# Optimization experiments

Hardware: AMD Instinct MI355X
Metric: run time of the kernel (lower is better)

Reference implementation:

```python
import jax, jax.numpy as jnp
import numpy as np

L, I, H = 4, 256, 512          # layers, input_size, hidden_size
SH, LH, GH = 4, 2, 2            # short/long/global heads
NH, HD, FF = SH + LH + GH, H // (SH + LH + GH), 2 * H
S, B = 1024, 8                  # seq (AST nodes), batch
EPS = 1e-5
NEG = -1e9


def _ln(x, g, b):
    m = jnp.mean(x, axis=-1, keepdims=True)
    v = jnp.var(x, axis=-1, keepdims=True)
    return (x - m) * jax.lax.rsqrt(v + EPS) * g + b


def setup_inputs() -> dict:
    key = jax.random.key(0)
    ks = jax.random.split(key, 10)
    w = lambda k, shape: jax.random.normal(k, shape, jnp.float32) * 0.02
    return {
        "nodes": jax.random.normal(ks[0], (S, B, I), jnp.float32),
        "dist": jax.random.randint(ks[1], (B, S, S), 0, 5, jnp.int32),
        "dense_w": w(ks[2], (H, I)), "dense_b": jnp.zeros((H,), jnp.float32),
        "dense_ln_g": jnp.ones((H,), jnp.float32), "dense_ln_b": jnp.zeros((H,), jnp.float32),
        "qkv_w": w(ks[3], (L, 3 * H, H)), "qkv_b": jnp.zeros((L, 3 * H), jnp.float32),
        "out_w": w(ks[4], (L, H, H)), "out_b": jnp.zeros((L, H), jnp.float32),
        "ln1_g": jnp.ones((L, H), jnp.float32), "ln1_b": jnp.zeros((L, H), jnp.float32),
        "ffn_w1": w(ks[5], (L, FF, H)), "ffn_b1": jnp.zeros((L, FF), jnp.float32),
        "ffn_w2": w(ks[6], (L, H, FF)), "ffn_b2": jnp.zeros((L, H), jnp.float32),
        "ln2_g": jnp.ones((L, H), jnp.float32), "ln2_b": jnp.zeros((L, H), jnp.float32),
        "bn_g": jnp.ones((H,), jnp.float32), "bn_b": jnp.zeros((H,), jnp.float32),
    }


def _mask_bias(dist):
    # dist: [B,S,S] int -> additive bias [B,NH,S,S]
    short = (dist == 1)[:, None]                       # [B,1,S,S]
    longm = (dist >= 1)[:, None]
    globm = jnp.broadcast_to((dist[:, 0:1, :] >= 1)[:, None], (dist.shape[0], 1, S, S))
    allowed = jnp.concatenate([
        jnp.broadcast_to(short, (dist.shape[0], SH, S, S)),
        jnp.broadcast_to(longm, (dist.shape[0], LH, S, S)),
        jnp.broadcast_to(globm, (dist.shape[0], GH, S, S)),
    ], axis=1)
    allowed = allowed | jnp.eye(S, dtype=bool)
    return jnp.where(allowed, 0.0, NEG).astype(jnp.float32)


def _forward(nodes, dist, dense_w, dense_b, dense_ln_g, dense_ln_b,
             qkv_w, qkv_b, out_w, out_b, ln1_g, ln1_b,
             ffn_w1, ffn_b1, ffn_w2, ffn_b2, ln2_g, ln2_b, bn_g, bn_b):
    x = jnp.transpose(nodes, (1, 0, 2))                # [B,S,I]
    x = _ln(x @ dense_w.T + dense_b, dense_ln_g, dense_ln_b)  # [B,S,H]
    bias = _mask_bias(dist)                            # [B,NH,S,S]
    scale = 1.0 / np.sqrt(HD)

    def layer(x, p):
        (wqkv, bqkv, wo, bo, g1, b1, w1, bf1, w2, bf2, g2, b2) = p
        qkv = x @ wqkv.T + bqkv                        # [B,S,3H]
        q, k, v = jnp.split(qkv, 3, axis=-1)
        q = q.reshape(B, S, NH, HD).transpose(0, 2, 1, 3)
        k = k.reshape(B, S, NH, HD).transpose(0, 2, 1, 3)
        v = v.reshape(B, S, NH, HD).transpose(0, 2, 1, 3)
        scores = jnp.einsum('bhqd,bhkd->bhqk', q, k) * scale + bias
        attn = jax.nn.softmax(scores, axis=-1)
        o = jnp.einsum('bhqk,bhkd->bhqd', attn, v)
        o = o.transpose(0, 2, 1, 3).reshape(B, S, H) @ wo.T + bo
        x = _ln(x + o, g1, b1)
        f = jax.nn.relu(x @ w1.T + bf1) @ w2.T + bf2
        x = _ln(x + f, g2, b2)
        return x, None

    params = (qkv_w, qkv_b, out_w, out_b, ln1_g, ln1_b,
              ffn_w1, ffn_b1, ffn_w2, ffn_b2, ln2_g, ln2_b)
    x, _ = jax.lax.scan(layer, x, params)
    hidden = x[:, 0]                                   # first token -> [B,H]
    m = jnp.mean(hidden, axis=0)
    v = jnp.var(hidden, axis=0)
    return (hidden - m) * jax.lax.rsqrt(v + EPS) * bn_g + bn_b


def reference(nodes, dist, dense_w, dense_b, dense_ln_g, dense_ln_b,
              qkv_w, qkv_b, out_w, out_b, ln1_g, ln1_b,
              ffn_w1, ffn_b1, ffn_w2, ffn_b2, ln2_g, ln2_b, bn_g, bn_b):
    return _forward(nodes, dist, dense_w, dense_b, dense_ln_g, dense_ln_b,
                    qkv_w, qkv_b, out_w, out_b, ln1_g, ln1_b,
                    ffn_w1, ffn_b1, ffn_w2, ffn_b2, ln2_g, ln2_b, bn_g, bn_b)
```

## Files before the change

### kernel.cpp

```cpp
#include <hip/hip_runtime.h>
#include <hip/hip_bf16.h>
#include <math.h>

#define LAYERS 4
#define IDIM 256
#define HDIM 512
#define NH 8
#define HD 64
#define FF 1024
#define SEQ 1024
#define BATCH 8
#define EPS 1e-5f

typedef __attribute__((ext_vector_type(8))) short short8;
typedef __attribute__((ext_vector_type(4))) short short4v;
typedef __attribute__((ext_vector_type(4))) float f32x4;
typedef unsigned long long u64;

__device__ __forceinline__ short f2bf(float f) {
    unsigned u = __float_as_uint(f);
    u = (u + 0x7FFFu + ((u >> 16) & 1u)) >> 16;
    return (short)u;
}
__device__ __forceinline__ float bf2f(short s) {
    return __uint_as_float(((unsigned)(unsigned short)s) << 16);
}
__device__ __forceinline__ void gll16(const void* g, void* l) {
    __builtin_amdgcn_global_load_lds(
        (const __attribute__((address_space(1))) unsigned int*)g,
        (__attribute__((address_space(3))) unsigned int*)l, 16, 0, 0);
}

__global__ __launch_bounds__(256) void cvt_bf16(const float* __restrict__ in,
                                                short* __restrict__ out) {
    size_t i = ((size_t)blockIdx.x * 256 + threadIdx.x) * 4;
    f32x4 f = *(const f32x4*)(in + i);
    short4v o = {f2bf(f[0]), f2bf(f[1]), f2bf(f[2]), f2bf(f[3])};
    *(short4v*)(out + i) = o;
}

__global__ __launch_bounds__(256) void transpose_nodes(const float* __restrict__ nodes,
                                                       short* __restrict__ xt) {
    size_t idx = ((size_t)blockIdx.x * 256 + threadIdx.x) * 4;
    int i  = idx & (IDIM - 1);
    int sb = idx >> 8;
    int b  = sb & (BATCH - 1);
    int s  = sb >> 3;
    f32x4 f = *(const f32x4*)(nodes + idx);
    short4v o = {f2bf(f[0]), f2bf(f[1]), f2bf(f[2]), f2bf(f[3])};
    *(short4v*)(xt + ((size_t)b * SEQ + s) * IDIM + i) = o;
}

__global__ __launch_bounds__(256) void build_masks(const int* __restrict__ dist,
                                                   u64* __restrict__ mS,
                                                   u64* __restrict__ mL,
                                                   u64* __restrict__ mG) {
    int t = blockIdx.x * 256 + threadIdx.x;
    int w = t & 15, q = (t >> 4) & 1023, b = t >> 14;
    const int* dp = dist + ((size_t)b * SEQ + q) * SEQ + w * 64;
    u64 bs = 0, bl = 0;
    for (int i = 0; i < 64; i++) {
        int d = dp[i];
        bs |= (u64)(d == 1) << i;
        bl |= (u64)(d >= 1) << i;
    }
    mS[((size_t)b * SEQ + q) * 16 + w] = bs;
    mL[((size_t)b * SEQ + q) * 16 + w] = bl;
    if (q == 0) mG[b * 16 + w] = bl;
}

template<int BM>
__global__ __launch_bounds__(256, 2)
void gemm_bf16(const short* __restrict__ A, const short* __restrict__ W,
               const float* __restrict__ bias, short* __restrict__ C,
               int M, int N, int K, int relu) {
    __shared__ __align__(16) short As[BM * 64];
    __shared__ __align__(16) short Ws[128 * 64];
    const int tid = threadIdx.x;
    const int w = tid >> 6, lane = tid & 63;
    const int l15 = lane & 15, quad = lane >> 4;
    const int m0 = blockIdx.y * BM, n0 = blockIdx.x * 128;

    constexpr int NI = (BM == 128) ? 4 : 2;
    const int wm = (BM == 128) ? (w >> 1) * 64 : 0;
    const int wn = (BM == 128) ? (w & 1) * 64 : w * 32;

    f32x4 acc[4][NI];
#pragma unroll
    for (int mi = 0; mi < 4; mi++)
#pragma unroll
        for (int ni = 0; ni < NI; ni++) acc[mi][ni] = (f32x4){0.f, 0.f, 0.f, 0.f};

    const int r_in = lane >> 3;
    const int c8   = lane & 7;

    for (int k0 = 0; k0 < K; k0 += 64) {
#pragma unroll
        for (int rep = 0; rep < BM * 8 / 256; rep++) {
            int chunk = rep * 4 + w;
            int row = chunk * 8 + r_in;
            const short* src = A + (size_t)(m0 + row) * K + k0 + ((c8 ^ (row & 7)) << 3);
            gll16(src, (char*)As + chunk * 1024);
        }
#pragma unroll
        for (int rep = 0; rep < 4; rep++) {
            int chunk = rep * 4 + w;
            int row = chunk * 8 + r_in;
            const short* src = W + (size_t)(n0 + row) * K + k0 + ((c8 ^ (row & 7)) << 3);
            gll16(src, (char*)Ws + chunk * 1024);
        }
        __syncthreads();
#pragma unroll
        for (int ks = 0; ks < 2; ks++) {
            short8 af[4], wf[NI];
            const int dblk = ks * 4 + quad;
#pragma unroll
            for (int mi = 0; mi < 4; mi++) {
                int row = wm + mi * 16 + l15;
                af[mi] = *(const short8*)((const char*)As + row * 128 + ((dblk ^ (row & 7)) << 4));
            }
#pragma unroll
            for (int ni = 0; ni < NI; ni++) {
                int row = wn + ni * 16 + l15;
                wf[ni] = *(const short8*)((const char*)Ws + row * 128 + ((dblk ^ (row & 7)) << 4));
            }
#pragma unroll
            for (int mi = 0; mi < 4; mi++)
#pragma unroll
                for (int ni = 0; ni < NI; ni++)
                    acc[mi][ni] = __builtin_amdgcn_mfma_f32_16x16x32_bf16(
                        af[mi], wf[ni], acc[mi][ni], 0, 0, 0);
        }
        __syncthreads();
    }
#pragma unroll
    for (int ni = 0; ni < NI; ni++) {
        int n = n0 + wn + ni * 16 + l15;
        float bz = bias[n];
#pragma unroll
        for (int mi = 0; mi < 4; mi++) {
#pragma unroll
            for (int r = 0; r < 4; r++) {
                int m = m0 + wm + mi * 16 + quad * 4 + r;
                float v = acc[mi][ni][r] + bz;
                if (relu) v = fmaxf(v, 0.f);
                C[(size_t)m * N + n] = f2bf(v);
            }
        }
    }
}

__global__ __launch_bounds__(256) void v_transpose(const short* __restrict__ qkv,
                                                   short* __restrict__ vt) {
    const int s0 = blockIdx.x * 64, h = blockIdx.y, b = blockIdx.z;
    __shared__ __align__(16) short T[64 * 72];
    const int tid = threadIdx.x;
#pragma unroll
    for (int rep = 0; rep < 2; rep++) {
        int item = tid + rep * 256;
        int sl = item >> 3, c = item & 7;
        short8 v = *(const short8*)(qkv + ((size_t)(b * SEQ + s0 + sl) * 1536) + 1024 + h * 64 + c * 8);
        *(short8*)(T + sl * 72 + c * 8) = v;
    }
    __syncthreads();
    int d = tid & 63, g = tid >> 6;
    short8 o0, o1;
#pragma unroll
    for (int i = 0; i < 8; i++) o0[i] = T[(g * 16 + i) * 72 + d];
#pragma unroll
    for (int i = 0; i < 8; i++) o1[i] = T[(g * 16 + 8 + i) * 72 + d];
    short* dst = vt + ((size_t)((b * NH + h) * HD + d) * SEQ) + s0 + g * 16;
    *(short8*)dst = o0;
    *(short8*)(dst + 8) = o1;
}

#define EXP2SC 0.18033688011112042f
__global__ __launch_bounds__(256, 3)
void attn_mfma(const short* __restrict__ qkv, const short* __restrict__ vt,
               const u64* __restrict__ maskS, const u64* __restrict__ maskL,
               const u64* __restrict__ maskG, short* __restrict__ out) {
    const int tid = threadIdx.x;
    const int w = tid >> 6, lane = tid & 63, l15 = lane & 15, quad = lane >> 4;
    const int p = blockIdx.x;
    const int g_ = (p & 7) + 8 * (p >> 7);
    const int qt = (p >> 3) & 15;
    const int b = g_ >> 3, h = g_ & 7;
    const int q = qt * 64 + w * 16 + l15;

    __shared__ __align__(16) short Ks[64 * 64];
    __shared__ __align__(16) short Vs[64 * 64];

    short8 qf[2];
    {
        const short* qrow = qkv + ((size_t)(b * SEQ + q) * 1536) + h * 64;
#pragma unroll
        for (int ks = 0; ks < 2; ks++)
            qf[ks] = *(const short8*)(qrow + ks * 32 + quad * 8);
    }
    const u64* mrow = (h < 4) ? (maskS + ((size_t)b * SEQ + q) * 16)
                   : (h < 6) ? (maskL + ((size_t)b * SEQ + q) * 16)
                   :           (maskG + (size_t)b * 16);

    f32x4 of[4];
#pragma unroll
    for (int mt = 0; mt < 4; mt++) of[mt] = (f32x4){0.f, 0.f, 0.f, 0.f};
    float lsum = 0.f;

    const int r_in = lane >> 3, c8 = lane & 7;
    for (int kt = 0; kt < SEQ; kt += 64) {
#pragma unroll
        for (int rep = 0; rep < 2; rep++) {
            int chunk = rep * 4 + w;
            int row = chunk * 8 + r_in;
            const short* ksrc = qkv + ((size_t)(b * SEQ + kt + row) * 1536) + 512 + h * 64 + ((c8 ^ (row & 7)) << 3);
            gll16(ksrc, (char*)Ks + chunk * 1024);
            const short* vsrc = vt + ((size_t)((b * NH + h) * HD + row) * SEQ) + kt + ((c8 ^ (row & 7)) << 3);
            gll16(vsrc, (char*)Vs + chunk * 1024);
        }
        __syncthreads();

        f32x4 sa[4];
#pragma unroll
        for (int g = 0; g < 4; g++) sa[g] = (f32x4){0.f, 0.f, 0.f, 0.f};
#pragma unroll
        for (int ks = 0; ks < 2; ks++) {
            const int dblk = ks * 4 + quad;
#pragma unroll
            for (int g = 0; g < 4; g++) {
                int row = g * 16 + l15;
                short8 kf = *(const short8*)((const char*)Ks + row * 128 + ((dblk ^ (row & 7)) << 4));
                sa[g] = __builtin_amdgcn_mfma_f32_16x16x32_bf16(kf, qf[ks], sa[g], 0, 0, 0);
            }
        }
        u64 mw = mrow[kt >> 6];
        if ((q >> 6) == (kt >> 6)) mw |= 1ull << (q & 63);
#if __has_builtin(__builtin_amdgcn_mfma_f32_16x16x16bf16_1k)
        short4v pfrag[4];
#pragma unroll
        for (int g = 0; g < 4; g++)
#pragma unroll
            for (int r = 0; r < 4; r++) {
                int key = g * 16 + quad * 4 + r;
                float bias = ((mw >> key) & 1ull) ? 0.f : -1e9f;
                float pv = exp2f(fmaf(sa[g][r], EXP2SC, bias));
                lsum += pv;
                pfrag[g][r] = f2bf(pv);
            }
#pragma unroll
        for (int g = 0; g < 4; g++) {
            const int blk = (g << 1) + (quad >> 1);
#pragma unroll
            for (int mt = 0; mt < 4; mt++) {
                int row = mt * 16 + l15;
                short4v vf = *(const short4v*)((const char*)Vs + row * 128 +
                                               ((blk ^ (row & 7)) << 4) + ((quad & 1) << 3));
                of[mt] = __builtin_amdgcn_mfma_f32_16x16x16bf16_1k(vf, pfrag[g], of[mt], 0, 0, 0);
            }
        }
#else
        float pp[4][4];
#pragma unroll
        for (int g = 0; g < 4; g++)
#pragma unroll
            for (int r = 0; r < 4; r++) {
                int key = g * 16 + quad * 4 + r;
                float bias = ((mw >> key) & 1ull) ? 0.f : -1e9f;
                float pv = exp2f(fmaf(sa[g][r], EXP2SC, bias));
                lsum += pv;
                pp[g][r] = pv;
            }
        short8 pf[2];
#pragma unroll
        for (int ks = 0; ks < 2; ks++) {
#pragma unroll
            for (int j = 0; j < 8; j++) {
                int src = (((quad & 1) * 2 + (j >> 2)) << 4) | l15;
                float lo = __shfl(pp[2 * ks][j & 3], src);
                float hi = __shfl(pp[2 * ks + 1][j & 3], src);
                pf[ks][j] = f2bf((quad < 2) ? lo : hi);
            }
        }
#pragma unroll
        for (int ks = 0; ks < 2; ks++) {
            const int dblk = ks * 4 + quad;
#pragma unroll
            for (int mt = 0; mt < 4; mt++) {
                int row = mt * 16 + l15;
                short8 vf = *(const short8*)((const char*)Vs + row * 128 + ((dblk ^ (row & 7)) << 4));
                of[mt] = __builtin_amdgcn_mfma_f32_16x16x32_bf16(vf, pf[ks], of[mt], 0, 0, 0);
            }
        }
#endif
        __syncthreads();
    }
    lsum += __shfl_xor(lsum, 16);
    lsum += __shfl_xor(lsum, 32);
    float inv = 1.f / lsum;
#pragma unroll
    for (int mt = 0; mt < 4; mt++) {
        short4v pk;
#pragma unroll
        for (int r = 0; r < 4; r++) pk[r] = f2bf(of[mt][r] * inv);
        *(short4v*)(out + ((size_t)(b * SEQ + q) * HDIM) + h * 64 + mt * 16 + quad * 4) = pk;
    }
}

__global__ __launch_bounds__(256) void ln_bf16(const short* __restrict__ x,
                                               const short* __restrict__ r,
                                               const float* __restrict__ g,
                                               const float* __restrict__ b,
                                               short* __restrict__ y) {
    const int wv = threadIdx.x >> 6, lane = threadIdx.x & 63;
    const size_t row = (size_t)blockIdx.x * 4 + wv;
    const size_t base = row * HDIM + lane * 8;
    short8 xv = *(const short8*)(x + base);
    float v[8];
#pragma unroll
    for (int i = 0; i < 8; i++) v[i] = bf2f(xv[i]);
    if (r) {
        short8 rv = *(const short8*)(r + base);
#pragma unroll
        for (int i = 0; i < 8; i++) v[i] += bf2f(rv[i]);
    }
    float s = 0.f, ss = 0.f;
#pragma unroll
    for (int i = 0; i < 8; i++) { s += v[i]; ss += v[i] * v[i]; }
#pragma unroll
    for (int off = 1; off < 64; off <<= 1) {
        s  += __shfl_xor(s, off);
        ss += __shfl_xor(ss, off);
    }
    const float mean = s * (1.f / HDIM);
    const float var  = ss * (1.f / HDIM) - mean * mean;
    const float inv  = rsqrtf(var + EPS);
    f32x4 g0 = *(const f32x4*)(g + lane * 8), g1 = *(const f32x4*)(g + lane * 8 + 4);
    f32x4 b0 = *(const f32x4*)(b + lane * 8), b1 = *(const f32x4*)(b + lane * 8 + 4);
    short8 o;
#pragma unroll
    for (int i = 0; i < 4; i++) o[i]     = f2bf((v[i]     - mean) * inv * g0[i] + b0[i]);
#pragma unroll
    for (int i = 0; i < 4; i++) o[i + 4] = f2bf((v[i + 4] - mean) * inv * g1[i] + b1[i]);
    *(short8*)(y + base) = o;
}

__global__ __launch_bounds__(256) void final_bn(const short* __restrict__ X,
                                                const float* __restrict__ g,
                                                const float* __restrict__ bb,
                                                float* __restrict__ out) {
    int h = blockIdx.x * 256 + threadIdx.x;
    if (h >= HDIM) return;
    float vals[BATCH];
    float m = 0.f;
#pragma unroll
    for (int b = 0; b < BATCH; b++) {
        vals[b] = bf2f(X[(size_t)b * SEQ * HDIM + h]);
        m += vals[b];
    }
    m *= (1.f / BATCH);
    float v = 0.f;
#pragma unroll
    for (int b = 0; b < BATCH; b++) { float d = vals[b] - m; v += d * d; }
    v *= (1.f / BATCH);
    float inv = rsqrtf(v + EPS);
#pragma unroll
    for (int b = 0; b < BATCH; b++)
        out[b * HDIM + h] = (vals[b] - m) * inv * g[h] + bb[h];
}

extern "C" void kernel_launch(void* const* d_in, const int* in_sizes, int n_in,
                              void* d_out, int out_size, void* d_ws, size_t ws_size,
                              hipStream_t stream) {
    const float* nodes      = (const float*)d_in[0];
    const int*   dist       = (const int*)  d_in[1];
    const float* dense_w    = (const float*)d_in[2];
    const float* dense_b    = (const float*)d_in[3];
    const float* dense_ln_g = (const float*)d_in[4];
    const float* dense_ln_b = (const float*)d_in[5];
    const float* qkv_w      = (const float*)d_in[6];
    const float* qkv_b      = (const float*)d_in[7];
    const float* out_w      = (const float*)d_in[8];
    const float* out_b      = (const float*)d_in[9];
    const float* ln1_g      = (const float*)d_in[10];
    const float* ln1_b      = (const float*)d_in[11];
    const float* ffn_w1     = (const float*)d_in[12];
    const float* ffn_b1     = (const float*)d_in[13];
    const float* ffn_w2     = (const float*)d_in[14];
    const float* ffn_b2     = (const float*)d_in[15];
    const float* ln2_g      = (const float*)d_in[16];
    const float* ln2_b      = (const float*)d_in[17];
    const float* bn_g       = (const float*)d_in[18];
    const float* bn_b       = (const float*)d_in[19];
    float* out = (float*)d_out;

    const int M = BATCH * SEQ;
    const size_t MB = 1024 * 1024;
    char* ws = (char*)d_ws;
    short* Wd   = (short*)(ws + 0 * MB);
    short* Wqkv = (short*)(ws + 1 * MB);
    short* Wo   = (short*)(ws + 9 * MB);
    short* W1   = (short*)(ws + 13 * MB);
    short* W2   = (short*)(ws + 18 * MB);
    u64*   mS   = (u64*)(ws + 23 * MB);
    u64*   mL   = (u64*)(ws + 24 * MB);
    u64*   mG   = (u64*)(ws + 25 * MB);
    short* X    = (short*)(ws + 26 * MB);
    short* QKV  = (short*)(ws + 34 * MB);
    short* Vt   = (short*)(ws + 58 * MB);
    short* AT   = (short*)(ws + 66 * MB);
    short* O2   = (short*)(ws + 74 * MB);
    short* XT   = QKV;
    short* F1   = QKV;
    short* F2   = AT;

    cvt_bf16<<<(HDIM * IDIM) / 1024, 256, 0, stream>>>(dense_w, Wd);
    cvt_bf16<<<(LAYERS * 3 * HDIM * HDIM) / 1024, 256, 0, stream>>>(qkv_w, Wqkv);
    cvt_bf16<<<(LAYERS * HDIM * HDIM) / 1024, 256, 0, stream>>>(out_w, Wo);
    cvt_bf16<<<(LAYERS * FF * HDIM) / 1024, 256, 0, stream>>>(ffn_w1, W1);
    cvt_bf16<<<(LAYERS * HDIM * FF) / 1024, 256, 0, stream>>>(ffn_w2, W2);

    transpose_nodes<<<(SEQ * BATCH * IDIM) / 1024, 256, 0, stream>>>(nodes, XT);
    build_masks<<<(BATCH * SEQ * 16) / 256, 256, 0, stream>>>(dist, mS, mL, mG);

    gemm_bf16<64><<<dim3(HDIM / 128, M / 64), 256, 0, stream>>>(XT, Wd, dense_b, O2,
                                                                M, HDIM, IDIM, 0);
    ln_bf16<<<M / 4, 256, 0, stream>>>(O2, nullptr, dense_ln_g, dense_ln_b, X);

    for (int l = 0; l < LAYERS; l++) {
        const short* wqkv = Wqkv + (size_t)l * 3 * HDIM * HDIM;
        const float* bqkv = qkv_b + (size_t)l * 3 * HDIM;
        const short* wo   = Wo + (size_t)l * HDIM * HDIM;
        const float* bo   = out_b + (size_t)l * HDIM;
        const short* w1   = W1 + (size_t)l * FF * HDIM;
        const float* b1   = ffn_b1 + (size_t)l * FF;
        const short* w2   = W2 + (size_t)l * HDIM * FF;
        const float* b2   = ffn_b2 + (size_t)l * HDIM;

        gemm_bf16<128><<<dim3(3 * HDIM / 128, M / 128), 256, 0, stream>>>(
            X, wqkv, bqkv, QKV, M, 3 * HDIM, HDIM, 0);
        v_transpose<<<dim3(SEQ / 64, NH, BATCH), 256, 0, stream>>>(QKV, Vt);
        attn_mfma<<<1024, 256, 0, stream>>>(QKV, Vt, mS, mL, mG, AT);
        gemm_bf16<64><<<dim3(HDIM / 128, M / 64), 256, 0, stream>>>(
            AT, wo, bo, O2, M, HDIM, HDIM, 0);
        ln_bf16<<<M / 4, 256, 0, stream>>>(X, O2, ln1_g + l * HDIM, ln1_b + l * HDIM, X);
        gemm_bf16<128><<<dim3(FF / 128, M / 128), 256, 0, stream>>>(
            X, w1, b1, F1, M, FF, HDIM, 1);
        gemm_bf16<64><<<dim3(HDIM / 128, M / 64), 256, 0, stream>>>(
            F1, w2, b2, F2, M, HDIM, FF, 0);
        ln_bf16<<<M / 4, 256, 0, stream>>>(X, F2, ln2_g + l * HDIM, ln2_b + l * HDIM, X);
    }
    final_bn<<<(HDIM + 255) / 256, 256, 0, stream>>>(X, bn_g, bn_b, out);
}
```

Before: 656.6 us.

## Fuse V transpose into QKV GEMM epilogue, merge weight casts, tune attention

The QKV GEMM epilogue now writes the V columns straight into the transposed, permuted Vt layout, so the separate v_transpose kernel and its round trip through memory go away. The five weight-cast launches become one launch, and mask building reads dist with vector int4 loads. Attention packs probabilities to bf16 by truncating with a byte permute instead of rounding, reads V with one wide LDS load per pair of MFMAs, and asks for higher occupancy in its launch bounds. The risks are register pressure at the higher occupancy, scattered short4 stores in the GEMM epilogue, and a small accuracy loss from truncating P.

Measured after the change: 645.0 us. Within noise of the previous version (-1.8%).

```diff
diff --git a/kernel.cpp b/kernel.cpp
--- a/kernel.cpp
+++ b/kernel.cpp
@@ -15,6 +15,8 @@
 typedef __attribute__((ext_vector_type(8))) short short8;
 typedef __attribute__((ext_vector_type(4))) short short4v;
 typedef __attribute__((ext_vector_type(4))) float f32x4;
+typedef __attribute__((ext_vector_type(4))) int int4v;
+typedef __attribute__((ext_vector_type(2))) unsigned int uint2v;
 typedef unsigned long long u64;
 
 __device__ __forceinline__ short f2bf(float f) {
@@ -31,12 +33,26 @@
         (__attribute__((address_space(3))) unsigned int*)l, 16, 0, 0);
 }
 
-__global__ __launch_bounds__(256) void cvt_bf16(const float* __restrict__ in,
-                                                short* __restrict__ out) {
+#define CVT_P0 131072u
+#define CVT_P1 3276800u
+#define CVT_P2 4325376u
+#define CVT_P3 6422528u
+#define CVT_TOT 8519680u
+__global__ __launch_bounds__(256) void cvt_all(const float* __restrict__ s0, short* __restrict__ d0,
+                                               const float* __restrict__ s1, short* __restrict__ d1,
+                                               const float* __restrict__ s2, short* __restrict__ d2,
+                                               const float* __restrict__ s3, short* __restrict__ d3,
+                                               const float* __restrict__ s4, short* __restrict__ d4) {
     size_t i = ((size_t)blockIdx.x * 256 + threadIdx.x) * 4;
-    f32x4 f = *(const f32x4*)(in + i);
+    const float* s; short* d; size_t off;
+    if (i < CVT_P0)      { s = s0; d = d0; off = i; }
+    else if (i < CVT_P1) { s = s1; d = d1; off = i - CVT_P0; }
+    else if (i < CVT_P2) { s = s2; d = d2; off = i - CVT_P1; }
+    else if (i < CVT_P3) { s = s3; d = d3; off = i - CVT_P2; }
+    else                 { s = s4; d = d4; off = i - CVT_P3; }
+    f32x4 f = *(const f32x4*)(s + off);
     short4v o = {f2bf(f[0]), f2bf(f[1]), f2bf(f[2]), f2bf(f[3])};
-    *(short4v*)(out + i) = o;
+    *(short4v*)(d + off) = o;
 }
 
 __global__ __launch_bounds__(256) void transpose_nodes(const float* __restrict__ nodes,
@@ -57,12 +73,16 @@
                                                    u64* __restrict__ mG) {
     int t = blockIdx.x * 256 + threadIdx.x;
     int w = t & 15, q = (t >> 4) & 1023, b = t >> 14;
-    const int* dp = dist + ((size_t)b * SEQ + q) * SEQ + w * 64;
+    const int4v* dp = (const int4v*)(dist + ((size_t)b * SEQ + q) * SEQ + w * 64);
     u64 bs = 0, bl = 0;
-    for (int i = 0; i < 64; i++) {
-        int d = dp[i];
-        bs |= (u64)(d == 1) << i;
-        bl |= (u64)(d >= 1) << i;
+#pragma unroll
+    for (int i = 0; i < 16; i++) {
+        int4v d = dp[i];
+#pragma unroll
+        for (int j = 0; j < 4; j++) {
+            bs |= (u64)(d[j] == 1) << (i * 4 + j);
+            bl |= (u64)(d[j] >= 1) << (i * 4 + j);
+        }
     }
     mS[((size_t)b * SEQ + q) * 16 + w] = bs;
     mL[((size_t)b * SEQ + q) * 16 + w] = bl;
@@ -73,7 +93,7 @@
 __global__ __launch_bounds__(256, 2)
 void gemm_bf16(const short* __restrict__ A, const short* __restrict__ W,
                const float* __restrict__ bias, short* __restrict__ C,
-               int M, int N, int K, int relu) {
+               short* __restrict__ vt, int M, int N, int K, int relu) {
     __shared__ __align__(16) short As[BM * 64];
     __shared__ __align__(16) short Ws[128 * 64];
     const int tid = threadIdx.x;
@@ -133,49 +153,46 @@
         }
         __syncthreads();
     }
-#pragma unroll
-    for (int ni = 0; ni < NI; ni++) {
-        int n = n0 + wn + ni * 16 + l15;
-        float bz = bias[n];
-#pragma unroll
-        for (int mi = 0; mi < 4; mi++) {
-#pragma unroll
-            for (int r = 0; r < 4; r++) {
-                int m = m0 + wm + mi * 16 + quad * 4 + r;
-                float v = acc[mi][ni][r] + bz;
-                if (relu) v = fmaxf(v, 0.f);
-                C[(size_t)m * N + n] = f2bf(v);
-            }
-        }
-    }
-}
-
-__global__ __launch_bounds__(256) void v_transpose(const short* __restrict__ qkv,
-                                                   short* __restrict__ vt) {
-    const int s0 = blockIdx.x * 64, h = blockIdx.y, b = blockIdx.z;
-    __shared__ __align__(16) short T[64 * 72];
-    const int tid = threadIdx.x;
-#pragma unroll
-    for (int rep = 0; rep < 2; rep++) {
-        int item = tid + rep * 256;
-        int sl = item >> 3, c = item & 7;
-        short8 v = *(const short8*)(qkv + ((size_t)(b * SEQ + s0 + sl) * 1536) + 1024 + h * 64 + c * 8);
-        *(short8*)(T + sl * 72 + c * 8) = v;
-    }
-    __syncthreads();
-    int d = tid & 63, g = tid >> 6;
-    short8 o0, o1;
-#pragma unroll
-    for (int i = 0; i < 8; i++) o0[i] = T[(g * 16 + i) * 72 + d];
-#pragma unroll
-    for (int i = 0; i < 8; i++) o1[i] = T[(g * 16 + 8 + i) * 72 + d];
-    short* dst = vt + ((size_t)((b * NH + h) * HD + d) * SEQ) + s0 + g * 16;
-    *(short8*)dst = o0;
-    *(short8*)(dst + 8) = o1;
+    if (vt && n0 >= 1024) {
+#pragma unroll
+        for (int ni = 0; ni < NI; ni++) {
+            int n = n0 + wn + ni * 16 + l15;
+            int d = n - 1024, h = d >> 6, dd = d & 63;
+            float bz = bias[n];
+#pragma unroll
+            for (int mi = 0; mi < 4; mi++) {
+                int mbase = m0 + wm + mi * 16 + quad * 4;
+                int b = mbase >> 10, s = mbase & 1023;
+                int tile = s >> 6, j = (s & 63) >> 2;
+                size_t off = ((size_t)(b * NH + h) * HD + dd) * SEQ
+                           + tile * 64 + (j & 7) * 8 + (j >> 3) * 4;
+                short4v pk;
+#pragma unroll
+                for (int r = 0; r < 4; r++) pk[r] = f2bf(acc[mi][ni][r] + bz);
+                *(short4v*)(vt + off) = pk;
+            }
+        }
+    } else {
+#pragma unroll
+        for (int ni = 0; ni < NI; ni++) {
+            int n = n0 + wn + ni * 16 + l15;
+            float bz = bias[n];
+#pragma unroll
+            for (int mi = 0; mi < 4; mi++) {
+#pragma unroll
+                for (int r = 0; r < 4; r++) {
+                    int m = m0 + wm + mi * 16 + quad * 4 + r;
+                    float v = acc[mi][ni][r] + bz;
+                    if (relu) v = fmaxf(v, 0.f);
+                    C[(size_t)m * N + n] = f2bf(v);
+                }
+            }
+        }
+    }
 }
 
 #define EXP2SC 0.18033688011112042f
-__global__ __launch_bounds__(256, 3)
+__global__ __launch_bounds__(256, 4)
 void attn_mfma(const short* __restrict__ qkv, const short* __restrict__ vt,
                const u64* __restrict__ maskS, const u64* __restrict__ maskL,
                const u64* __restrict__ maskG, short* __restrict__ out) {
@@ -234,63 +251,35 @@
         }
         u64 mw = mrow[kt >> 6];
         if ((q >> 6) == (kt >> 6)) mw |= 1ull << (q & 63);
-#if __has_builtin(__builtin_amdgcn_mfma_f32_16x16x16bf16_1k)
         short4v pfrag[4];
 #pragma unroll
-        for (int g = 0; g < 4; g++)
+        for (int g = 0; g < 4; g++) {
+            float pv[4];
 #pragma unroll
             for (int r = 0; r < 4; r++) {
                 int key = g * 16 + quad * 4 + r;
                 float bias = ((mw >> key) & 1ull) ? 0.f : -1e9f;
-                float pv = exp2f(fmaf(sa[g][r], EXP2SC, bias));
-                lsum += pv;
-                pfrag[g][r] = f2bf(pv);
-            }
-#pragma unroll
-        for (int g = 0; g < 4; g++) {
-            const int blk = (g << 1) + (quad >> 1);
+                pv[r] = exp2f(fmaf(sa[g][r], EXP2SC, bias));
+                lsum += pv[r];
+            }
+            uint2v pk;
+            pk[0] = __builtin_amdgcn_perm(__float_as_uint(pv[1]), __float_as_uint(pv[0]), 0x07060302u);
+            pk[1] = __builtin_amdgcn_perm(__float_as_uint(pv[3]), __float_as_uint(pv[2]), 0x07060302u);
+            pfrag[g] = __builtin_bit_cast(short4v, pk);
+        }
+#pragma unroll
+        for (int g01 = 0; g01 < 2; g01++) {
+            const int u = g01 * 4 + quad;
 #pragma unroll
             for (int mt = 0; mt < 4; mt++) {
                 int row = mt * 16 + l15;
-                short4v vf = *(const short4v*)((const char*)Vs + row * 128 +
-                                               ((blk ^ (row & 7)) << 4) + ((quad & 1) << 3));
-                of[mt] = __builtin_amdgcn_mfma_f32_16x16x16bf16_1k(vf, pfrag[g], of[mt], 0, 0, 0);
-            }
-        }
-#else
-        float pp[4][4];
-#pragma unroll
-        for (int g = 0; g < 4; g++)
-#pragma unroll
-            for (int r = 0; r < 4; r++) {
-                int key = g * 16 + quad * 4 + r;
-                float bias = ((mw >> key) & 1ull) ? 0.f : -1e9f;
-                float pv = exp2f(fmaf(sa[g][r], EXP2SC, bias));
-                lsum += pv;
-                pp[g][r] = pv;
-            }
-        short8 pf[2];
-#pragma unroll
-        for (int ks = 0; ks < 2; ks++) {
-#pragma unroll
-            for (int j = 0; j < 8; j++) {
-                int src = (((quad & 1) * 2 + (j >> 2)) << 4) | l15;
-                float lo = __shfl(pp[2 * ks][j & 3], src);
-                float hi = __shfl(pp[2 * ks + 1][j & 3], src);
-                pf[ks][j] = f2bf((quad < 2) ? lo : hi);
-            }
-        }
-#pragma unroll
-        for (int ks = 0; ks < 2; ks++) {
-            const int dblk = ks * 4 + quad;
-#pragma unroll
-            for (int mt = 0; mt < 4; mt++) {
-                int row = mt * 16 + l15;
-                short8 vf = *(const short8*)((const char*)Vs + row * 128 + ((dblk ^ (row & 7)) << 4));
-                of[mt] = __builtin_amdgcn_mfma_f32_16x16x32_bf16(vf, pf[ks], of[mt], 0, 0, 0);
-            }
-        }
-#endif
+                short8 vv = *(const short8*)((const char*)Vs + row * 128 + ((u ^ (row & 7)) << 4));
+                short4v vlo = {vv[0], vv[1], vv[2], vv[3]};
+                short4v vhi = {vv[4], vv[5], vv[6], vv[7]};
+                of[mt] = __builtin_amdgcn_mfma_f32_16x16x16bf16_1k(vlo, pfrag[g01], of[mt], 0, 0, 0);
+                of[mt] = __builtin_amdgcn_mfma_f32_16x16x16bf16_1k(vhi, pfrag[g01 + 2], of[mt], 0, 0, 0);
+            }
+        }
         __syncthreads();
     }
     lsum += __shfl_xor(lsum, 16);
@@ -412,17 +401,13 @@
     short* F1   = QKV;
     short* F2   = AT;
 
-    cvt_bf16<<<(HDIM * IDIM) / 1024, 256, 0, stream>>>(dense_w, Wd);
-    cvt_bf16<<<(LAYERS * 3 * HDIM * HDIM) / 1024, 256, 0, stream>>>(qkv_w, Wqkv);
-    cvt_bf16<<<(LAYERS * HDIM * HDIM) / 1024, 256, 0, stream>>>(out_w, Wo);
-    cvt_bf16<<<(LAYERS * FF * HDIM) / 1024, 256, 0, stream>>>(ffn_w1, W1);
-    cvt_bf16<<<(LAYERS * HDIM * FF) / 1024, 256, 0, stream>>>(ffn_w2, W2);
-
+    cvt_all<<<CVT_TOT / 1024, 256, 0, stream>>>(dense_w, Wd, qkv_w, Wqkv,
+                                                out_w, Wo, ffn_w1, W1, ffn_w2, W2);
     transpose_nodes<<<(SEQ * BATCH * IDIM) / 1024, 256, 0, stream>>>(nodes, XT);
     build_masks<<<(BATCH * SEQ * 16) / 256, 256, 0, stream>>>(dist, mS, mL, mG);
 
-    gemm_bf16<64><<<dim3(HDIM / 128, M / 64), 256, 0, stream>>>(XT, Wd, dense_b, O2,
-                                                                M, HDIM, IDIM, 0);
+    gemm_bf16<64><<<dim3(HDIM / 128, M / 64), 256, 0, stream>>>(
+        XT, Wd, dense_b, O2, nullptr, M, HDIM, IDIM, 0);
     ln_bf16<<<M / 4, 256, 0, stream>>>(O2, nullptr, dense_ln_g, dense_ln_b, X);
 
     for (int l = 0; l < LAYERS; l++) {
@@ -436,16 +421,15 @@
         const float* b2   = ffn_b2 + (size_t)l * HDIM;
 
         gemm_bf16<128><<<dim3(3 * HDIM / 128, M / 128), 256, 0, stream>>>(
-            X, wqkv, bqkv, QKV, M, 3 * HDIM, HDIM, 0);
-        v_transpose<<<dim3(SEQ / 64, NH, BATCH), 256, 0, stream>>>(QKV, Vt);
+            X, wqkv, bqkv, QKV, Vt, M, 3 * HDIM, HDIM, 0);
         attn_mfma<<<1024, 256, 0, stream>>>(QKV, Vt, mS, mL, mG, AT);
         gemm_bf16<64><<<dim3(HDIM / 128, M / 64), 256, 0, stream>>>(
-            AT, wo, bo, O2, M, HDIM, HDIM, 0);
+            AT, wo, bo, O2, nullptr, M, HDIM, HDIM, 0);
         ln_bf16<<<M / 4, 256, 0, stream>>>(X, O2, ln1_g + l * HDIM, ln1_b + l * HDIM, X);
         gemm_bf16<128><<<dim3(FF / 128, M / 128), 256, 0, stream>>>(
-            X, w1, b1, F1, M, FF, HDIM, 1);
+            X, w1, b1, F1, nullptr, M, FF, HDIM, 1);
         gemm_bf16<64><<<dim3(HDIM / 128, M / 64), 256, 0, stream>>>(
-            F1, w2, b2, F2, M, HDIM, FF, 0);
+            F1, w2, b2, F2, nullptr, M, HDIM, FF, 0);
         ln_bf16<<<M / 4, 256, 0, stream>>>(X, F2, ln2_g + l * HDIM, ln2_b + l * HDIM, X);
     }
     final_bn<<<(HDIM + 255) / 256, 256, 0, stream>>>(X, bn_g, bn_b, out);
```
